# Performance work log

Hardware: AMD Instinct MI355X
Metric: run time of the kernel (lower is better)

The kernel has to match this reference:

```python
import jax, jax.numpy as jnp
import numpy as np
from jax import lax

B, S, D, NH, K = 4, 2048, 1024, 16, 3
EPS = 1e-6


def custom_layernorm(x, gamma, beta):
    # torch-style: std with ddof=1, eps added to std (not var)
    mean = jnp.mean(x, axis=-1, keepdims=True)
    var = jnp.sum((x - mean) ** 2, axis=-1, keepdims=True) / (x.shape[-1] - 1)
    std = jnp.sqrt(var)
    return gamma * ((x - mean) / (std + EPS)) + beta


def setup_inputs() -> dict:
    key = jax.random.key(0)
    ks = jax.random.split(key, 10)
    s = 1.0 / np.sqrt(D)
    return {
        "x": jax.random.normal(ks[0], (B, S, D), jnp.float32),
        "Wq": jax.random.normal(ks[1], (D, D), jnp.float32) * s,
        "bq": jax.random.normal(ks[2], (D,), jnp.float32) * 0.02,
        "Wk": jax.random.normal(ks[3], (D, D), jnp.float32) * s,
        "Wv": jax.random.normal(ks[4], (D, D), jnp.float32) * s,
        "bv": jax.random.normal(ks[5], (D,), jnp.float32) * 0.02,
        "conv_w": jax.random.normal(ks[6], (D, D // NH, K), jnp.float32) * (1.0 / np.sqrt((D // NH) * K)),
        "conv_b": jax.random.normal(ks[7], (D,), jnp.float32) * 0.02,
        "gamma": jnp.ones((D,), jnp.float32),
        "beta": jnp.zeros((D,), jnp.float32),
        "Wo": jax.random.normal(ks[8], (D, D), jnp.float32) * s,
        "bo": jax.random.normal(ks[9], (D,), jnp.float32) * 0.02,
    }


def reference(x, Wq, bq, Wk, Wv, bv, conv_w, conv_b, gamma, beta, Wo, bo):
    d = x.shape[-1]
    groups = d // conv_w.shape[1]
    pad = conv_w.shape[2] // 2

    q = x @ Wq + bq
    k = x @ Wk  # key has no bias
    v = x @ Wv + bv

    # grouped conv1d over sequence dim (NCW layout)
    xc = jnp.transpose(x, (0, 2, 1))  # [B, D, S]
    conv_out = lax.conv_general_dilated(
        xc, conv_w, window_strides=(1,), padding=[(pad, pad)],
        feature_group_count=groups,
        dimension_numbers=("NCH", "OIH", "NCH"),
    ) + conv_b[None, :, None]
    conv_out = jnp.transpose(conv_out, (0, 2, 1))  # [B, S, D]
    conv_out = custom_layernorm(conv_out, gamma, beta)  # dropout = identity (eval)

    scale = 1.0 / jnp.sqrt(jnp.asarray(d, x.dtype))
    scores = jnp.einsum("bqd,bkd->bqk", q, k) * scale  # [B, S, S]
    attn = jax.nn.softmax(scores, axis=-1)
    attention_out = jnp.einsum("bqk,bkd->bqd", attn, v)

    combined = custom_layernorm(conv_out + attention_out, gamma, beta)
    return combined @ Wo + bo + x
```

## Files before the change

kernel.cpp:

```cpp
#include <hip/hip_runtime.h>
#include <cstdint>


#define DEV __device__ __forceinline__

typedef unsigned short u16;
typedef __attribute__((ext_vector_type(8))) short bf16x8;
typedef __attribute__((ext_vector_type(4))) float f32x4;

static const int Sn = 2048, Dn = 1024;

DEV float bf2f(u16 u) { union { unsigned int i; float f; } w; w.i = ((unsigned int)u) << 16; return w.f; }
DEV u16 f2bf(float f) {
  union { float f; unsigned int i; } w; w.f = f;
  unsigned int x = w.i;
  return (u16)((x + 0x7FFFu + ((x >> 16) & 1u)) >> 16);
}

DEV void gload_lds16(const u16* gsrc, u16* lds_dst) {
  __builtin_amdgcn_global_load_lds(
      (const __attribute__((address_space(1))) void*)gsrc,
      (__attribute__((address_space(3))) void*)lds_dst,
      16, 0, 0);
}

DEV float block_allreduce_sum(float v, float* red, int tid) {
  #pragma unroll
  for (int o = 32; o > 0; o >>= 1) v += __shfl_down(v, o, 64);
  __syncthreads();
  if ((tid & 63) == 0) red[tid >> 6] = v;
  __syncthreads();
  return red[0] + red[1] + red[2] + red[3];
}

DEV float block_allreduce_max(float v, float* red, int tid) {
  #pragma unroll
  for (int o = 32; o > 0; o >>= 1) v = fmaxf(v, __shfl_down(v, o, 64));
  __syncthreads();
  if ((tid & 63) == 0) red[tid >> 6] = v;
  __syncthreads();
  return fmaxf(fmaxf(red[0], red[1]), fmaxf(red[2], red[3]));
}

DEV void ln_row(const u16* __restrict__ a, const u16* __restrict__ b2,
                const float* __restrict__ gamma, const float* __restrict__ beta,
                u16* __restrict__ out, long row, int tid, float* red) {
  long base = row * Dn + tid * 4;
  ushort4 av = *(const ushort4*)&a[base];
  float v0 = bf2f(av.x), v1 = bf2f(av.y), v2 = bf2f(av.z), v3 = bf2f(av.w);
  if (b2) {
    ushort4 bv4 = *(const ushort4*)&b2[base];
    v0 += bf2f(bv4.x); v1 += bf2f(bv4.y); v2 += bf2f(bv4.z); v3 += bf2f(bv4.w);
  }
  float s = block_allreduce_sum(v0 + v1 + v2 + v3, red, tid);
  float mean = s * (1.0f / 1024.0f);
  float d0 = v0 - mean, d1 = v1 - mean, d2 = v2 - mean, d3 = v3 - mean;
  float sq = block_allreduce_sum(d0 * d0 + d1 * d1 + d2 * d2 + d3 * d3, red, tid);
  float inv = 1.0f / (sqrtf(sq * (1.0f / 1023.0f)) + 1e-6f);
  float4 gv = *(const float4*)&gamma[tid * 4];
  float4 bev = *(const float4*)&beta[tid * 4];
  ushort4 o;
  o.x = f2bf(gv.x * d0 * inv + bev.x);
  o.y = f2bf(gv.y * d1 * inv + bev.y);
  o.z = f2bf(gv.z * d2 * inv + bev.z);
  o.w = f2bf(gv.w * d3 * inv + bev.w);
  *(ushort4*)&out[base] = o;
}

__global__ __launch_bounds__(256)
void prep_all(const float* __restrict__ Wq, const float* __restrict__ Wk,
              const float* __restrict__ Wv, const float* __restrict__ Wo,
              u16* __restrict__ wT,
              const float* __restrict__ bq, const float* __restrict__ bv,
              float* __restrict__ qkvb,
              const float* __restrict__ x, u16* __restrict__ xb) {
  __shared__ u16 sm[64][68];
  int blk = blockIdx.x;
  int tid = threadIdx.x;
  if (blk < 1024) {
    int w = blk >> 8, t = blk & 255;
    const float* src = (w == 0) ? Wq : (w == 1) ? Wk : (w == 2) ? Wv : Wo;
    u16* dst = wT + (size_t)w * 1048576u;
    int i0 = (t >> 4) << 6, j0 = (t & 15) << 6;
    int tx = tid & 15, r0 = tid >> 4;
    #pragma unroll
    for (int rr = r0; rr < 64; rr += 16) {
      float4 v = *(const float4*)&src[(long)(i0 + rr) * 1024 + j0 + tx * 4];
      sm[rr][tx*4+0] = f2bf(v.x); sm[rr][tx*4+1] = f2bf(v.y);
      sm[rr][tx*4+2] = f2bf(v.z); sm[rr][tx*4+3] = f2bf(v.w);
    }
    __syncthreads();
    #pragma unroll
    for (int cc = r0; cc < 64; cc += 16) {
      ushort4 o;
      o.x = sm[tx*4+0][cc]; o.y = sm[tx*4+1][cc];
      o.z = sm[tx*4+2][cc]; o.w = sm[tx*4+3][cc];
      *(ushort4*)&dst[(long)(j0 + cc) * 1024 + i0 + tx * 4] = o;
    }
  } else if (blk == 1024) {
    for (int j = tid; j < 3072; j += 256) {
      float v = 0.0f;
      if (j < 1024) v = bq[j];
      else if (j >= 2048) v = bv[j - 2048];
      qkvb[j] = v;
    }
  } else {
    int i = (blk - 1025) * 1024 + tid * 4;
    float4 v = *(const float4*)&x[i];
    ushort4 o;
    o.x = f2bf(v.x); o.y = f2bf(v.y); o.z = f2bf(v.z); o.w = f2bf(v.w);
    *(ushort4*)&xb[i] = o;
  }
}

__global__ __launch_bounds__(512, 2)
void gemm8(const u16* __restrict__ A, long Abs, int lda,
           const u16* __restrict__ B, long Bbs, int ldb,
           u16* __restrict__ C0, u16* __restrict__ C1, int zsplit,
           long Cbs, int ldc, int K, float scale,
           const float* __restrict__ bias, int bias_bs) {
  extern __shared__ u16 lds[];
  int tid = threadIdx.x;
  int w = tid >> 6, ln = tid & 63;
  int quad = ln >> 4, lm = ln & 15;
  int wr = w >> 2, wc = w & 3;
  long m0 = (long)blockIdx.x * 256, n0 = (long)blockIdx.y * 256;
  int z = blockIdx.z;
  A += (long)z * Abs;
  B += (long)z * Bbs;
  u16* C = (z < zsplit) ? C0 + (long)z * Cbs : C1 + (long)(z - zsplit) * Cbs;

  int sg = ((ln & 7) ^ (ln >> 3)) * 8;
  int row0 = w * 8 + (ln >> 3);
  const u16* As0 = A + (m0 + row0) * (long)lda + sg;
  const u16* As1 = As0 + 64 * (long)lda;
  const u16* Bs0 = B + (n0 + row0) * (long)ldb + sg;
  const u16* Bs1 = Bs0 + 64 * (long)ldb;
  u16* dA = lds + w * 512;
  u16* dB = lds + 16384 + w * 512;

  int rA = wr * 16 + lm;
  int rB = wc * 16 + lm;
  int g0 = (quad ^ (lm & 7)) * 8;
  int g1 = ((4 + quad) ^ (lm & 7)) * 8;

#define STGA(buf, h, k0) do { \
    gload_lds16(As0 + (long)(h) * 128 * lda + (k0), dA + (buf) * 32768 + (h) * 8192); \
    gload_lds16(As1 + (long)(h) * 128 * lda + (k0), dA + (buf) * 32768 + (h) * 8192 + 4096); } while (0)
#define STGB(buf, h, k0) do { \
    gload_lds16(Bs0 + (long)(h) * 128 * ldb + (k0), dB + (buf) * 32768 + (h) * 8192); \
    gload_lds16(Bs1 + (long)(h) * 128 * ldb + (k0), dB + (buf) * 32768 + (h) * 8192 + 4096); } while (0)
#define LDA_F(ab, mi, kk) (*(const bf16x8*)&lds[(ab) + ((mi) * 32 + rA) * 64 + ((kk) ? g1 : g0)])
#define LDB_F(bb, ni, kk) (*(const bf16x8*)&lds[(bb) + ((ni) * 64 + rB) * 64 + ((kk) ? g1 : g0)])
#define MFMA(a, b, c) __builtin_amdgcn_mfma_f32_16x16x32_bf16(a, b, c, 0, 0, 0)

  f32x4 acc[8][4] = {};
  bf16x8 bfr[4][2];
  int nt = K >> 6;

  STGB(0, 0, 0); STGB(0, 1, 0); STGA(0, 0, 0); STGA(0, 1, 0);
  asm volatile("s_waitcnt vmcnt(2)" ::: "memory");
  __builtin_amdgcn_sched_barrier(0);
  __builtin_amdgcn_s_barrier();

  for (int t = 0; t < nt; ++t) {
    int buf = t & 1;
    int abase = buf * 32768, bbase = abase + 16384;
    int nbuf = buf ^ 1;
    int kn = (t + 1) << 6;
    bool more = (t + 1 < nt);

    {
      #pragma unroll
      for (int ni = 0; ni < 4; ni++) {
        bfr[ni][0] = LDB_F(bbase, ni, 0);
        bfr[ni][1] = LDB_F(bbase, ni, 1);
      }
      bf16x8 a00 = LDA_F(abase, 0, 0), a01 = LDA_F(abase, 0, 1);
      bf16x8 a10 = LDA_F(abase, 1, 0), a11 = LDA_F(abase, 1, 1);
      if (more) STGB(nbuf, 0, kn);
      __builtin_amdgcn_s_barrier();
      __builtin_amdgcn_s_setprio(1);
      #pragma unroll
      for (int ni = 0; ni < 4; ni++) {
        acc[0][ni] = MFMA(a00, bfr[ni][0], acc[0][ni]);
        acc[0][ni] = MFMA(a01, bfr[ni][1], acc[0][ni]);
        acc[1][ni] = MFMA(a10, bfr[ni][0], acc[1][ni]);
        acc[1][ni] = MFMA(a11, bfr[ni][1], acc[1][ni]);
      }
      __builtin_amdgcn_s_setprio(0);
      __builtin_amdgcn_s_barrier();
    }
    {
      bf16x8 a00 = LDA_F(abase, 2, 0), a01 = LDA_F(abase, 2, 1);
      bf16x8 a10 = LDA_F(abase, 3, 0), a11 = LDA_F(abase, 3, 1);
      if (more) STGB(nbuf, 1, kn);
      __builtin_amdgcn_s_barrier();
      __builtin_amdgcn_s_setprio(1);
      #pragma unroll
      for (int ni = 0; ni < 4; ni++) {
        acc[2][ni] = MFMA(a00, bfr[ni][0], acc[2][ni]);
        acc[2][ni] = MFMA(a01, bfr[ni][1], acc[2][ni]);
        acc[3][ni] = MFMA(a10, bfr[ni][0], acc[3][ni]);
        acc[3][ni] = MFMA(a11, bfr[ni][1], acc[3][ni]);
      }
      __builtin_amdgcn_s_setprio(0);
      if (more) asm volatile("s_waitcnt vmcnt(4)" ::: "memory");
      else      asm volatile("s_waitcnt vmcnt(0)" ::: "memory");
      __builtin_amdgcn_sched_barrier(0);
      __builtin_amdgcn_s_barrier();
    }
    {
      bf16x8 a00 = LDA_F(abase, 4, 0), a01 = LDA_F(abase, 4, 1);
      bf16x8 a10 = LDA_F(abase, 5, 0), a11 = LDA_F(abase, 5, 1);
      if (more) STGA(nbuf, 0, kn);
      __builtin_amdgcn_s_barrier();
      __builtin_amdgcn_s_setprio(1);
      #pragma unroll
      for (int ni = 0; ni < 4; ni++) {
        acc[4][ni] = MFMA(a00, bfr[ni][0], acc[4][ni]);
        acc[4][ni] = MFMA(a01, bfr[ni][1], acc[4][ni]);
        acc[5][ni] = MFMA(a10, bfr[ni][0], acc[5][ni]);
        acc[5][ni] = MFMA(a11, bfr[ni][1], acc[5][ni]);
      }
      __builtin_amdgcn_s_setprio(0);
      __builtin_amdgcn_s_barrier();
    }
    {
      bf16x8 a00 = LDA_F(abase, 6, 0), a01 = LDA_F(abase, 6, 1);
      bf16x8 a10 = LDA_F(abase, 7, 0), a11 = LDA_F(abase, 7, 1);
      if (more) STGA(nbuf, 1, kn);
      __builtin_amdgcn_s_barrier();
      __builtin_amdgcn_s_setprio(1);
      #pragma unroll
      for (int ni = 0; ni < 4; ni++) {
        acc[6][ni] = MFMA(a00, bfr[ni][0], acc[6][ni]);
        acc[6][ni] = MFMA(a01, bfr[ni][1], acc[6][ni]);
        acc[7][ni] = MFMA(a10, bfr[ni][0], acc[7][ni]);
        acc[7][ni] = MFMA(a11, bfr[ni][1], acc[7][ni]);
      }
      __builtin_amdgcn_s_setprio(0);
      if (more) {
        asm volatile("s_waitcnt vmcnt(2)" ::: "memory");
        __builtin_amdgcn_sched_barrier(0);
      }
      __builtin_amdgcn_s_barrier();
    }
  }

  #pragma unroll
  for (int mi = 0; mi < 8; mi++) {
    #pragma unroll
    for (int ni = 0; ni < 4; ni++) {
      int col = (int)n0 + ni * 64 + wc * 16 + lm;
      float bvv = bias ? bias[(long)z * bias_bs + col] : 0.0f;
      #pragma unroll
      for (int r = 0; r < 4; r++) {
        long rowg = m0 + mi * 32 + wr * 16 + quad * 4 + r;
        C[rowg * (long)ldc + col] = f2bf(acc[mi][ni][r] * scale + bvv);
      }
    }
  }
#undef STGA
#undef STGB
#undef LDA_F
#undef LDB_F
#undef MFMA
}

template<typename CT>
__global__ __launch_bounds__(256, 2)
void gemm_nt(const u16* __restrict__ A, const u16* __restrict__ A2, long Abs, int lda,
             const u16* __restrict__ B, long Bbs, int ldb,
             CT* __restrict__ C, CT* __restrict__ C2, long Cbs, int ldc,
             int zsplit, int K, float scale,
             const float* __restrict__ bias, int bias_bs,
             const float* __restrict__ res, long Rbs, int ldr) {
  __shared__ u16 sA[2][128 * 32];
  __shared__ u16 sB[2][128 * 32];
  int tid = threadIdx.x;
  int lane = tid & 63, wv = tid >> 6;
  int quad = lane >> 4, lm = lane & 15;
  int wr = wv >> 1, wc = wv & 1;
  long m0 = (long)blockIdx.x * 128, n0 = (long)blockIdx.y * 128;
  int z = blockIdx.z;
  if (z >= zsplit) { A = A2 + (long)(z - zsplit) * Abs; C = C2 + (long)(z - zsplit) * Cbs; }
  else             { A = A  + (long)z * Abs;            C = C  + (long)z * Cbs; }
  B += (long)z * Bbs;
  if (res) res += (long)z * Rbs;

  f32x4 acc[4][4] = {};

  int srow = wv * 16 + (lane >> 2);
  int sch = (lane & 3) * 8;
  const u16* Ap = A + (m0 + srow) * (long)lda + sch;
  const u16* Bp = B + (n0 + srow) * (long)ldb + sch;
  const int lofs = wv * 16 * 32;

  for (int k0 = 0; k0 < K; k0 += 64) {
    #pragma unroll
    for (int h = 0; h < 2; h++) {
      int kh = k0 + h * 32;
      gload_lds16(Ap + kh, &sA[h][lofs]);
      gload_lds16(Ap + 64 * (long)lda + kh, &sA[h][lofs + 64 * 32]);
      gload_lds16(Bp + kh, &sB[h][lofs]);
      gload_lds16(Bp + 64 * (long)ldb + kh, &sB[h][lofs + 64 * 32]);
    }
    __syncthreads();
    #pragma unroll
    for (int h = 0; h < 2; h++) {
      bf16x8 af[4], bfr[4];
      #pragma unroll
      for (int mi = 0; mi < 4; mi++)
        af[mi] = *(const bf16x8*)&sA[h][(wr * 64 + mi * 16 + lm) * 32 + quad * 8];
      #pragma unroll
      for (int ni = 0; ni < 4; ni++)
        bfr[ni] = *(const bf16x8*)&sB[h][(wc * 64 + ni * 16 + lm) * 32 + quad * 8];
      #pragma unroll
      for (int mi = 0; mi < 4; mi++)
        #pragma unroll
        for (int ni = 0; ni < 4; ni++)
          acc[mi][ni] = __builtin_amdgcn_mfma_f32_16x16x32_bf16(af[mi], bfr[ni], acc[mi][ni], 0, 0, 0);
    }
    __syncthreads();
  }

  #pragma unroll
  for (int mi = 0; mi < 4; mi++) {
    #pragma unroll
    for (int ni = 0; ni < 4; ni++) {
      int col = (int)n0 + wc * 64 + ni * 16 + lm;
      float bv = bias ? bias[(long)z * bias_bs + col] : 0.0f;
      #pragma unroll
      for (int r = 0; r < 4; r++) {
        long rowg = m0 + wr * 64 + mi * 16 + quad * 4 + r;
        float v = acc[mi][ni][r] * scale + bv;
        if (res) v += res[rowg * (long)ldr + col];
        if constexpr (sizeof(CT) == 2) C[rowg * (long)ldc + col] = f2bf(v);
        else                           C[rowg * (long)ldc + col] = v;
      }
    }
  }
}

__global__ __launch_bounds__(256, 2)
void post_qkv(int ngemm,
              const u16* __restrict__ Qb, const u16* __restrict__ Kb,
              u16* __restrict__ Pd, u16* __restrict__ Pw,
              const u16* __restrict__ Vb, u16* __restrict__ vt) {
  __shared__ u16 smem[2 * 2 * 128 * 32];
  int blk = blockIdx.x;
  int tid = threadIdx.x;
  if (blk < ngemm) {
    u16* sA0 = smem;
    u16* sB0 = smem + 2 * 128 * 32;
    int lane = tid & 63, wv = tid >> 6;
    int quad = lane >> 4, lm = lane & 15;
    int wr = wv >> 1, wc = wv & 1;
    int z = blk >> 8;
    long m0 = (long)(blk & 15) * 128, n0 = (long)((blk >> 4) & 15) * 128;
    const u16* A = Qb + (long)z * Sn * Dn;
    const u16* B = Kb + (long)z * Sn * Dn;
    u16* C = (z < 2) ? Pd + (long)z * Sn * Sn : Pw + (long)(z - 2) * Sn * Sn;

    f32x4 acc[4][4] = {};
    int srow = wv * 16 + (lane >> 2);
    int sch = (lane & 3) * 8;
    const u16* Ap = A + (m0 + srow) * 1024 + sch;
    const u16* Bp = B + (n0 + srow) * 1024 + sch;
    const int lofs = wv * 16 * 32;

    for (int k0 = 0; k0 < 1024; k0 += 64) {
      #pragma unroll
      for (int h = 0; h < 2; h++) {
        int kh = k0 + h * 32;
        gload_lds16(Ap + kh, &sA0[h * 128 * 32 + lofs]);
        gload_lds16(Ap + 64 * 1024 + kh, &sA0[h * 128 * 32 + lofs + 64 * 32]);
        gload_lds16(Bp + kh, &sB0[h * 128 * 32 + lofs]);
        gload_lds16(Bp + 64 * 1024 + kh, &sB0[h * 128 * 32 + lofs + 64 * 32]);
      }
      __syncthreads();
      #pragma unroll
      for (int h = 0; h < 2; h++) {
        bf16x8 af[4], bfr[4];
        #pragma unroll
        for (int mi = 0; mi < 4; mi++)
          af[mi] = *(const bf16x8*)&sA0[h * 128 * 32 + (wr * 64 + mi * 16 + lm) * 32 + quad * 8];
        #pragma unroll
        for (int ni = 0; ni < 4; ni++)
          bfr[ni] = *(const bf16x8*)&sB0[h * 128 * 32 + (wc * 64 + ni * 16 + lm) * 32 + quad * 8];
        #pragma unroll
        for (int mi = 0; mi < 4; mi++)
          #pragma unroll
          for (int ni = 0; ni < 4; ni++)
            acc[mi][ni] = __builtin_amdgcn_mfma_f32_16x16x32_bf16(af[mi], bfr[ni], acc[mi][ni], 0, 0, 0);
      }
      __syncthreads();
    }
    #pragma unroll
    for (int mi = 0; mi < 4; mi++) {
      #pragma unroll
      for (int ni = 0; ni < 4; ni++) {
        int col = (int)n0 + wc * 64 + ni * 16 + lm;
        #pragma unroll
        for (int r = 0; r < 4; r++) {
          long rowg = m0 + wr * 64 + mi * 16 + quad * 4 + r;
          C[rowg * 2048 + col] = f2bf(acc[mi][ni][r] * 0.03125f);
        }
      }
    }
  } else {
    u16 (*sm)[68] = (u16(*)[68])smem;
    int t = blk - ngemm;
    int b = t >> 9, r = t & 511;
    int j0 = (r & 15) << 6, i0 = ((r >> 4) & 31) << 6;
    const u16* s = Vb + (long)b * Sn * Dn;
    u16* d = vt + (long)b * Dn * Sn;
    int tx = tid & 15, r0 = tid >> 4;
    #pragma unroll
    for (int rr = r0; rr < 64; rr += 16) {
      ushort4 v = *(const ushort4*)&s[(long)(i0 + rr) * 1024 + j0 + tx * 4];
      sm[rr][tx*4+0] = v.x; sm[rr][tx*4+1] = v.y; sm[rr][tx*4+2] = v.z; sm[rr][tx*4+3] = v.w;
    }
    __syncthreads();
    #pragma unroll
    for (int cc = r0; cc < 64; cc += 16) {
      ushort4 o;
      o.x = sm[tx*4+0][cc]; o.y = sm[tx*4+1][cc];
      o.z = sm[tx*4+2][cc]; o.w = sm[tx*4+3][cc];
      *(ushort4*)&d[(long)(j0 + cc) * 2048 + i0 + tx * 4] = o;
    }
  }
}

__global__ __launch_bounds__(256)
void smax_conv(u16* __restrict__ pa, u16* __restrict__ pb, int rowsplit,
               int nsm, int nconv,
               const float* __restrict__ x, const float* __restrict__ cw,
               const float* __restrict__ cb, u16* __restrict__ convo,
               const u16* __restrict__ Vb, u16* __restrict__ vt) {
  __shared__ u16 smem[22160];
  __shared__ float red[4];
  int blk = blockIdx.x;
  int tid = threadIdx.x;
  if (blk < nsm) {
    long row = blk;
    u16* p = (row < rowsplit) ? pa + row * 2048 : pb + (row - rowsplit) * 2048;
    ushort4 a = *(const ushort4*)&p[tid * 8];
    ushort4 b = *(const ushort4*)&p[tid * 8 + 4];
    float f0 = bf2f(a.x), f1 = bf2f(a.y), f2 = bf2f(a.z), f3 = bf2f(a.w);
    float f4 = bf2f(b.x), f5 = bf2f(b.y), f6 = bf2f(b.z), f7 = bf2f(b.w);
    float m = fmaxf(fmaxf(fmaxf(f0, f1), fmaxf(f2, f3)),
                    fmaxf(fmaxf(f4, f5), fmaxf(f6, f7)));
    m = block_allreduce_max(m, red, tid);
    float e0 = __expf(f0 - m), e1 = __expf(f1 - m), e2 = __expf(f2 - m), e3 = __expf(f3 - m);
    float e4 = __expf(f4 - m), e5 = __expf(f5 - m), e6 = __expf(f6 - m), e7 = __expf(f7 - m);
    float s = block_allreduce_sum(e0 + e1 + e2 + e3 + e4 + e5 + e6 + e7, red, tid);
    float inv = 1.0f / s;
    ushort4 o1, o2;
    o1.x = f2bf(e0 * inv); o1.y = f2bf(e1 * inv); o1.z = f2bf(e2 * inv); o1.w = f2bf(e3 * inv);
    o2.x = f2bf(e4 * inv); o2.y = f2bf(e5 * inv); o2.z = f2bf(e6 * inv); o2.w = f2bf(e7 * inv);
    *(ushort4*)&p[tid * 8] = o1;
    *(ushort4*)&p[tid * 8 + 4] = o2;
  } else if (blk < nsm + nconv) {
    u16 (*sx)[72] = (u16(*)[72])smem;
    u16 (*sw)[200] = (u16(*)[200])(smem + 9360);
    int r = blk - nsm;
    int s0 = (r & 15) * 128;
    int g = (r >> 4) & 15;
    int b = r >> 8;
    int lane = tid & 63, wv = tid >> 6;
    int quad = lane >> 4, lm = lane & 15;
    for (int idx = tid; idx < 64 * 192; idx += 256) {
      int oc = idx / 192, k = idx - oc * 192;
      int t = k >> 6, i = k & 63;
      sw[oc][k] = f2bf(cw[((long)(g * 64 + oc)) * 192 + i * 3 + t]);
    }
    for (int idx = tid; idx < 130 * 16; idx += 256) {
      int rr = idx >> 4, c4 = (idx & 15) * 4;
      int s = s0 - 1 + rr;
      ushort4 v;
      if (s >= 0 && s < Sn) {
        float4 f = *(const float4*)&x[((long)b * Sn + s) * Dn + g * 64 + c4];
        v.x = f2bf(f.x); v.y = f2bf(f.y); v.z = f2bf(f.z); v.w = f2bf(f.w);
      } else { v.x = 0; v.y = 0; v.z = 0; v.w = 0; }
      *(ushort4*)&sx[rr][c4] = v;
    }
    __syncthreads();
    f32x4 acc[2][4] = {};
    #pragma unroll
    for (int ks = 0; ks < 6; ks++) {
      int t = ks >> 1;
      int i0 = (ks & 1) * 32 + quad * 8;
      bf16x8 a0 = *(const bf16x8*)&sx[wv * 32 + lm + t][i0];
      bf16x8 a1 = *(const bf16x8*)&sx[wv * 32 + 16 + lm + t][i0];
      #pragma unroll
      for (int nf = 0; nf < 4; nf++) {
        bf16x8 bf = *(const bf16x8*)&sw[nf * 16 + lm][ks * 32 + quad * 8];
        acc[0][nf] = __builtin_amdgcn_mfma_f32_16x16x32_bf16(a0, bf, acc[0][nf], 0, 0, 0);
        acc[1][nf] = __builtin_amdgcn_mfma_f32_16x16x32_bf16(a1, bf, acc[1][nf], 0, 0, 0);
      }
    }
    #pragma unroll
    for (int mi = 0; mi < 2; mi++) {
      #pragma unroll
      for (int nf = 0; nf < 4; nf++) {
        int col = g * 64 + nf * 16 + lm;
        float bias = cb[col];
        #pragma unroll
        for (int rr = 0; rr < 4; rr++) {
          int row = wv * 32 + mi * 16 + quad * 4 + rr;
          convo[((long)b * Sn + s0 + row) * Dn + col] = f2bf(acc[mi][nf][rr] + bias);
        }
      }
    }
  } else {
    u16 (*sm)[68] = (u16(*)[68])smem;
    int t = blk - nsm - nconv;
    int b = t >> 9, r = t & 511;
    int j0 = (r & 15) << 6, i0 = ((r >> 4) & 31) << 6;
    const u16* s = Vb + (long)b * Sn * Dn;
    u16* d = vt + (long)b * Dn * Sn;
    int tx = tid & 15, r0 = tid >> 4;
    #pragma unroll
    for (int rr = r0; rr < 64; rr += 16) {
      ushort4 v = *(const ushort4*)&s[(long)(i0 + rr) * 1024 + j0 + tx * 4];
      sm[rr][tx*4+0] = v.x; sm[rr][tx*4+1] = v.y; sm[rr][tx*4+2] = v.z; sm[rr][tx*4+3] = v.w;
    }
    __syncthreads();
    #pragma unroll
    for (int cc = r0; cc < 64; cc += 16) {
      ushort4 o;
      o.x = sm[tx*4+0][cc]; o.y = sm[tx*4+1][cc];
      o.z = sm[tx*4+2][cc]; o.w = sm[tx*4+3][cc];
      *(ushort4*)&d[(long)(j0 + cc) * 2048 + i0 + tx * 4] = o;
    }
  }
}

__global__ __launch_bounds__(256, 2)
void pv_ln(int npv,
           const u16* __restrict__ Pd, const u16* __restrict__ Pw,
           const u16* __restrict__ vt, u16* __restrict__ attn,
           u16* __restrict__ conv,
           const float* __restrict__ gamma, const float* __restrict__ beta) {
  __shared__ u16 smem[2 * 2 * 128 * 32];
  __shared__ float red[4];
  int blk = blockIdx.x;
  int tid = threadIdx.x;
  if (blk < npv) {
    u16* sA0 = smem;
    u16* sB0 = smem + 2 * 128 * 32;
    int lane = tid & 63, wv = tid >> 6;
    int quad = lane >> 4, lm = lane & 15;
    int wr = wv >> 1, wc = wv & 1;
    int z = blk >> 7;
    long m0 = (long)(blk & 15) * 128, n0 = (long)((blk >> 4) & 7) * 128;
    const u16* A = (z < 2) ? Pd + (long)z * Sn * Sn : Pw + (long)(z - 2) * Sn * Sn;
    const u16* B = vt + (long)z * Dn * Sn;
    u16* C = attn + (long)z * Sn * Dn;

    f32x4 acc[4][4] = {};
    int srow = wv * 16 + (lane >> 2);
    int sch = (lane & 3) * 8;
    const u16* Ap = A + (m0 + srow) * 2048 + sch;
    const u16* Bp = B + (n0 + srow) * 2048 + sch;
    const int lofs = wv * 16 * 32;

    for (int k0 = 0; k0 < 2048; k0 += 64) {
      #pragma unroll
      for (int h = 0; h < 2; h++) {
        int kh = k0 + h * 32;
        gload_lds16(Ap + kh, &sA0[h * 128 * 32 + lofs]);
        gload_lds16(Ap + 64 * 2048 + kh, &sA0[h * 128 * 32 + lofs + 64 * 32]);
        gload_lds16(Bp + kh, &sB0[h * 128 * 32 + lofs]);
        gload_lds16(Bp + 64 * 2048 + kh, &sB0[h * 128 * 32 + lofs + 64 * 32]);
      }
      __syncthreads();
      #pragma unroll
      for (int h = 0; h < 2; h++) {
        bf16x8 af[4], bfr[4];
        #pragma unroll
        for (int mi = 0; mi < 4; mi++)
          af[mi] = *(const bf16x8*)&sA0[h * 128 * 32 + (wr * 64 + mi * 16 + lm) * 32 + quad * 8];
        #pragma unroll
        for (int ni = 0; ni < 4; ni++)
          bfr[ni] = *(const bf16x8*)&sB0[h * 128 * 32 + (wc * 64 + ni * 16 + lm) * 32 + quad * 8];
        #pragma unroll
        for (int mi = 0; mi < 4; mi++)
          #pragma unroll
          for (int ni = 0; ni < 4; ni++)
            acc[mi][ni] = __builtin_amdgcn_mfma_f32_16x16x32_bf16(af[mi], bfr[ni], acc[mi][ni], 0, 0, 0);
      }
      __syncthreads();
    }
    #pragma unroll
    for (int mi = 0; mi < 4; mi++) {
      #pragma unroll
      for (int ni = 0; ni < 4; ni++) {
        int col = (int)n0 + wc * 64 + ni * 16 + lm;
        #pragma unroll
        for (int r = 0; r < 4; r++) {
          long rowg = m0 + wr * 64 + mi * 16 + quad * 4 + r;
          C[rowg * 1024 + col] = f2bf(acc[mi][ni][r]);
        }
      }
    }
  } else {
    long row = blk - npv;
    ln_row(conv, nullptr, gamma, beta, conv, row, tid, red);
  }
}

__global__ __launch_bounds__(256)
void ln_kernel(const u16* __restrict__ a, const u16* __restrict__ b2,
               const float* __restrict__ gamma, const float* __restrict__ beta,
               u16* __restrict__ out) {
  __shared__ float red[4];
  ln_row(a, b2, gamma, beta, out, blockIdx.x, threadIdx.x, red);
}

static const size_t OFF_WT    = 0;
static const size_t OFF_QKVB  = 8ull << 20;
static const size_t OFF_Q     = 9ull << 20;
static const size_t OFF_K     = 25ull << 20;
static const size_t OFF_V     = 41ull << 20;
static const size_t OFF_PW    = 57ull << 20;

extern "C" void kernel_launch(void* const* d_in, const int* in_sizes, int n_in,
                              void* d_out, int out_size, void* d_ws, size_t ws_size,
                              hipStream_t stream) {
  const float* x     = (const float*)d_in[0];
  const float* Wq    = (const float*)d_in[1];
  const float* bq    = (const float*)d_in[2];
  const float* Wk    = (const float*)d_in[3];
  const float* Wv    = (const float*)d_in[4];
  const float* bv    = (const float*)d_in[5];
  const float* cw    = (const float*)d_in[6];
  const float* cb    = (const float*)d_in[7];
  const float* gamma = (const float*)d_in[8];
  const float* beta  = (const float*)d_in[9];
  const float* Wo    = (const float*)d_in[10];
  const float* bo    = (const float*)d_in[11];
  float* out = (float*)d_out;
  char* ws = (char*)d_ws;

  u16*   wT    = (u16*)(ws + OFF_WT);
  float* qkvb  = (float*)(ws + OFF_QKVB);
  u16*   Qb    = (u16*)(ws + OFF_Q);
  u16*   Kb    = (u16*)(ws + OFF_K);
  u16*   Vb    = (u16*)(ws + OFF_V);
  u16*   Pw    = (u16*)(ws + OFF_PW);
  u16*   xb    = (u16*)d_out;
  u16*   Pd    = (u16*)d_out;
  u16*   vt    = (u16*)d_out + 8388608;
  u16*   attn  = Qb;
  u16*   combined = Kb;
  const long PBS = (long)Sn * Sn;

  static int gemm8_attr = 0;
  if (!gemm8_attr) {
    hipFuncSetAttribute((const void*)gemm8,
                        hipFuncAttributeMaxDynamicSharedMemorySize, 131072);
    gemm8_attr = 1;
  }

  dim3 tb(256);
  dim3 tb8(512);

  prep_all<<<dim3(9217), tb, 0, stream>>>(Wq, Wk, Wv, Wo, wT, bq, bv, qkvb, x, xb);
  gemm8<<<dim3(32, 4, 3), tb8, 131072, stream>>>(
      xb, 0, 1024, wT, 1048576, 1024,
      Qb, (u16*)nullptr, 99, 8388608, 1024,
      1024, 1.0f, qkvb, 1024);

  if (ws_size >= (73ull << 20)) {
    u16* conv = Kb;
    gemm8<<<dim3(8, 8, 4), tb8, 131072, stream>>>(
        Qb, (long)Sn * Dn, 1024, Kb, (long)Sn * Dn, 1024,
        Pd, Pw, 2, PBS, 2048,
        1024, 0.03125f, nullptr, 0);
    smax_conv<<<dim3(8192 + 1024 + 2048), tb, 0, stream>>>(
        Pd, Pw, 4096, 8192, 1024, x, cw, cb, conv, Vb, vt);
    pv_ln<<<dim3(512 + 8192), tb, 0, stream>>>(512, Pd, Pw, vt, attn, conv,
                                               gamma, beta);
    ln_kernel<<<dim3(8192), tb, 0, stream>>>(conv, attn, gamma, beta, combined);
  } else {
    u16* conv = Vb;
    post_qkv<<<dim3(2048), tb, 0, stream>>>(0, Qb, Kb, Pd, Pw, Vb, vt);
    for (int c = 0; c < 2; c++) {
      long off = (long)c * 2 * Sn * Dn;
      gemm_nt<u16><<<dim3(16, 16, 2), tb, 0, stream>>>(
          Qb + off, nullptr, (long)Sn * Dn, 1024, Kb + off, (long)Sn * Dn, 1024,
          Pd, (u16*)nullptr, PBS, 2048,
          99, 1024, 0.03125f, nullptr, 0, nullptr, 0, 0);
      smax_conv<<<dim3(4096 + (c == 0 ? 1024 : 0)), tb, 0, stream>>>(
          Pd, Pd, 4096, 4096, (c == 0 ? 1024 : 0), x, cw, cb, conv, Vb, vt);
      gemm_nt<u16><<<dim3(16, 8, 2), tb, 0, stream>>>(
          Pd, nullptr, PBS, 2048, vt + off, (long)Dn * Sn, 2048,
          attn + off, (u16*)nullptr, (long)Sn * Dn, 1024,
          99, 2048, 1.0f, nullptr, 0, nullptr, 0, 0);
    }
    ln_kernel<<<dim3(8192), tb, 0, stream>>>(conv, nullptr, gamma, beta, conv);
    ln_kernel<<<dim3(8192), tb, 0, stream>>>(conv, attn, gamma, beta, combined);
  }

  gemm_nt<float><<<dim3(64, 8, 1), tb, 0, stream>>>(
      combined, nullptr, 0, 1024, wT + 3u * 1048576u, 0, 1024,
      out, (float*)nullptr, 0, 1024,
      99, 1024, 1.0f, bo, 0, x, 0, 1024);
}
```

Measured before the change: 365.0 us.

## Software-pipeline gemm8 fragment loads across iterations and vectorize transposed epilogue stores

Restructures the gemm8 main loop so A fragments ping-pong between two register sets and the next tile's first A/B fragments are prefetched from LDS before the last MFMA cluster. Global-to-LDS staging is reordered with adjusted vmcnt waits. MFMA operands are swapped so the accumulators hold a transposed tile, which lets the epilogue use float4 bias loads and ushort4 stores instead of scalar stores. It adds register pressure and tighter synchronization ordering.

```diff
diff --git a/kernel.cpp b/kernel.cpp
--- a/kernel.cpp
+++ b/kernel.cpp
@@ -119,7 +119,8 @@
            u16* __restrict__ C0, u16* __restrict__ C1, int zsplit,
            long Cbs, int ldc, int K, float scale,
            const float* __restrict__ bias, int bias_bs) {
-  extern __shared__ u16 lds[];
+  extern __shared__ ulong2 lds_raw[];
+  u16* lds = (u16*)lds_raw;
   int tid = threadIdx.x;
   int w = tid >> 6, ln = tid & 63;
   int quad = ln >> 4, lm = ln & 15;
@@ -153,112 +154,105 @@
 #define LDA_F(ab, mi, kk) (*(const bf16x8*)&lds[(ab) + ((mi) * 32 + rA) * 64 + ((kk) ? g1 : g0)])
 #define LDB_F(bb, ni, kk) (*(const bf16x8*)&lds[(bb) + ((ni) * 64 + rB) * 64 + ((kk) ? g1 : g0)])
 #define MFMA(a, b, c) __builtin_amdgcn_mfma_f32_16x16x32_bf16(a, b, c, 0, 0, 0)
+#define CLUSTER(S, MLO, MHI) do { \
+    _Pragma("unroll") \
+    for (int ni = 0; ni < 4; ni++) { \
+      acc[MLO][ni] = MFMA(bfr[ni][0], S[0], acc[MLO][ni]); \
+      acc[MLO][ni] = MFMA(bfr[ni][1], S[1], acc[MLO][ni]); \
+      acc[MHI][ni] = MFMA(bfr[ni][0], S[2], acc[MHI][ni]); \
+      acc[MHI][ni] = MFMA(bfr[ni][1], S[3], acc[MHI][ni]); \
+    } } while (0)
+#define RDA(dst, base, mi) do { \
+    dst[0] = LDA_F(base, mi, 0); dst[1] = LDA_F(base, mi, 1); \
+    dst[2] = LDA_F(base, (mi) + 1, 0); dst[3] = LDA_F(base, (mi) + 1, 1); } while (0)
+#define VMCNT(n) do { asm volatile("s_waitcnt vmcnt(" #n ")" ::: "memory"); \
+    __builtin_amdgcn_sched_barrier(0); } while (0)
+#define BAR() __builtin_amdgcn_s_barrier()
 
   f32x4 acc[8][4] = {};
   bf16x8 bfr[4][2];
+  bf16x8 nb0[2], nb1[2];
+  bf16x8 aE[4], aO[4];
   int nt = K >> 6;
 
-  STGB(0, 0, 0); STGB(0, 1, 0); STGA(0, 0, 0); STGA(0, 1, 0);
-  asm volatile("s_waitcnt vmcnt(2)" ::: "memory");
-  __builtin_amdgcn_sched_barrier(0);
-  __builtin_amdgcn_s_barrier();
+  STGA(0, 0, 0); STGB(0, 0, 0); STGB(0, 1, 0); STGA(0, 1, 0);
+  VMCNT(4);
+  BAR();
+  {
+    RDA(aE, 0, 0);
+    bfr[0][0] = LDB_F(16384, 0, 0); bfr[0][1] = LDB_F(16384, 0, 1);
+    bfr[1][0] = LDB_F(16384, 1, 0); bfr[1][1] = LDB_F(16384, 1, 1);
+  }
+  VMCNT(2);
+  BAR();
 
   for (int t = 0; t < nt; ++t) {
     int buf = t & 1;
     int abase = buf * 32768, bbase = abase + 16384;
     int nbuf = buf ^ 1;
+    int nbabase = nbuf * 32768, nbbbase = nbabase + 16384;
     int kn = (t + 1) << 6;
     bool more = (t + 1 < nt);
 
-    {
-      #pragma unroll
-      for (int ni = 0; ni < 4; ni++) {
-        bfr[ni][0] = LDB_F(bbase, ni, 0);
-        bfr[ni][1] = LDB_F(bbase, ni, 1);
-      }
-      bf16x8 a00 = LDA_F(abase, 0, 0), a01 = LDA_F(abase, 0, 1);
-      bf16x8 a10 = LDA_F(abase, 1, 0), a11 = LDA_F(abase, 1, 1);
-      if (more) STGB(nbuf, 0, kn);
-      __builtin_amdgcn_s_barrier();
-      __builtin_amdgcn_s_setprio(1);
-      #pragma unroll
-      for (int ni = 0; ni < 4; ni++) {
-        acc[0][ni] = MFMA(a00, bfr[ni][0], acc[0][ni]);
-        acc[0][ni] = MFMA(a01, bfr[ni][1], acc[0][ni]);
-        acc[1][ni] = MFMA(a10, bfr[ni][0], acc[1][ni]);
-        acc[1][ni] = MFMA(a11, bfr[ni][1], acc[1][ni]);
-      }
-      __builtin_amdgcn_s_setprio(0);
-      __builtin_amdgcn_s_barrier();
-    }
-    {
-      bf16x8 a00 = LDA_F(abase, 2, 0), a01 = LDA_F(abase, 2, 1);
-      bf16x8 a10 = LDA_F(abase, 3, 0), a11 = LDA_F(abase, 3, 1);
-      if (more) STGB(nbuf, 1, kn);
-      __builtin_amdgcn_s_barrier();
-      __builtin_amdgcn_s_setprio(1);
-      #pragma unroll
-      for (int ni = 0; ni < 4; ni++) {
-        acc[2][ni] = MFMA(a00, bfr[ni][0], acc[2][ni]);
-        acc[2][ni] = MFMA(a01, bfr[ni][1], acc[2][ni]);
-        acc[3][ni] = MFMA(a10, bfr[ni][0], acc[3][ni]);
-        acc[3][ni] = MFMA(a11, bfr[ni][1], acc[3][ni]);
-      }
-      __builtin_amdgcn_s_setprio(0);
-      if (more) asm volatile("s_waitcnt vmcnt(4)" ::: "memory");
-      else      asm volatile("s_waitcnt vmcnt(0)" ::: "memory");
-      __builtin_amdgcn_sched_barrier(0);
-      __builtin_amdgcn_s_barrier();
-    }
-    {
-      bf16x8 a00 = LDA_F(abase, 4, 0), a01 = LDA_F(abase, 4, 1);
-      bf16x8 a10 = LDA_F(abase, 5, 0), a11 = LDA_F(abase, 5, 1);
-      if (more) STGA(nbuf, 0, kn);
-      __builtin_amdgcn_s_barrier();
-      __builtin_amdgcn_s_setprio(1);
-      #pragma unroll
-      for (int ni = 0; ni < 4; ni++) {
-        acc[4][ni] = MFMA(a00, bfr[ni][0], acc[4][ni]);
-        acc[4][ni] = MFMA(a01, bfr[ni][1], acc[4][ni]);
-        acc[5][ni] = MFMA(a10, bfr[ni][0], acc[5][ni]);
-        acc[5][ni] = MFMA(a11, bfr[ni][1], acc[5][ni]);
-      }
-      __builtin_amdgcn_s_setprio(0);
-      __builtin_amdgcn_s_barrier();
-    }
-    {
-      bf16x8 a00 = LDA_F(abase, 6, 0), a01 = LDA_F(abase, 6, 1);
-      bf16x8 a10 = LDA_F(abase, 7, 0), a11 = LDA_F(abase, 7, 1);
-      if (more) STGA(nbuf, 1, kn);
-      __builtin_amdgcn_s_barrier();
-      __builtin_amdgcn_s_setprio(1);
-      #pragma unroll
-      for (int ni = 0; ni < 4; ni++) {
-        acc[6][ni] = MFMA(a00, bfr[ni][0], acc[6][ni]);
-        acc[6][ni] = MFMA(a01, bfr[ni][1], acc[6][ni]);
-        acc[7][ni] = MFMA(a10, bfr[ni][0], acc[7][ni]);
-        acc[7][ni] = MFMA(a11, bfr[ni][1], acc[7][ni]);
-      }
-      __builtin_amdgcn_s_setprio(0);
-      if (more) {
-        asm volatile("s_waitcnt vmcnt(2)" ::: "memory");
-        __builtin_amdgcn_sched_barrier(0);
-      }
-      __builtin_amdgcn_s_barrier();
+    bfr[2][0] = LDB_F(bbase, 2, 0); bfr[2][1] = LDB_F(bbase, 2, 1);
+    bfr[3][0] = LDB_F(bbase, 3, 0); bfr[3][1] = LDB_F(bbase, 3, 1);
+    RDA(aO, abase, 2);
+    if (more) STGA(nbuf, 0, kn);
+    BAR();
+    __builtin_amdgcn_s_setprio(1);
+    CLUSTER(aE, 0, 1);
+    __builtin_amdgcn_s_setprio(0);
+    if (more) VMCNT(2); else VMCNT(0);
+    BAR();
+    RDA(aE, abase, 4);
+    if (more) STGB(nbuf, 0, kn);
+    BAR();
+    __builtin_amdgcn_s_setprio(1);
+    CLUSTER(aO, 2, 3);
+    __builtin_amdgcn_s_setprio(0);
+    BAR();
+    RDA(aO, abase, 6);
+    if (more) STGB(nbuf, 1, kn);
+    BAR();
+    __builtin_amdgcn_s_setprio(1);
+    CLUSTER(aE, 4, 5);
+    __builtin_amdgcn_s_setprio(0);
+    if (more) VMCNT(2);
+    BAR();
+    if (more) {
+      RDA(aE, nbabase, 0);
+      nb0[0] = LDB_F(nbbbase, 0, 0); nb0[1] = LDB_F(nbbbase, 0, 1);
+      nb1[0] = LDB_F(nbbbase, 1, 0); nb1[1] = LDB_F(nbbbase, 1, 1);
+      STGA(nbuf, 1, kn);
+    }
+    BAR();
+    __builtin_amdgcn_s_setprio(1);
+    CLUSTER(aO, 6, 7);
+    __builtin_amdgcn_s_setprio(0);
+    if (more) VMCNT(2);
+    BAR();
+    if (more) {
+      bfr[0][0] = nb0[0]; bfr[0][1] = nb0[1];
+      bfr[1][0] = nb1[0]; bfr[1][1] = nb1[1];
     }
   }
 
   #pragma unroll
   for (int mi = 0; mi < 8; mi++) {
+    long m = m0 + mi * 32 + wr * 16 + lm;
+    u16* Crow = C + m * (long)ldc;
     #pragma unroll
     for (int ni = 0; ni < 4; ni++) {
-      int col = (int)n0 + ni * 64 + wc * 16 + lm;
-      float bvv = bias ? bias[(long)z * bias_bs + col] : 0.0f;
-      #pragma unroll
-      for (int r = 0; r < 4; r++) {
-        long rowg = m0 + mi * 32 + wr * 16 + quad * 4 + r;
-        C[rowg * (long)ldc + col] = f2bf(acc[mi][ni][r] * scale + bvv);
-      }
+      int nb = (int)n0 + ni * 64 + wc * 16 + quad * 4;
+      float4 bv4;
+      if (bias) bv4 = *(const float4*)&bias[(long)z * bias_bs + nb];
+      else      bv4 = float4{0.0f, 0.0f, 0.0f, 0.0f};
+      ushort4 o;
+      o.x = f2bf(acc[mi][ni][0] * scale + bv4.x);
+      o.y = f2bf(acc[mi][ni][1] * scale + bv4.y);
+      o.z = f2bf(acc[mi][ni][2] * scale + bv4.z);
+      o.w = f2bf(acc[mi][ni][3] * scale + bv4.w);
+      *(ushort4*)&Crow[nb] = o;
     }
   }
 #undef STGA
@@ -266,6 +260,10 @@
 #undef LDA_F
 #undef LDB_F
 #undef MFMA
+#undef CLUSTER
+#undef RDA
+#undef VMCNT
+#undef BAR
 }
 
 template<typename CT>
```

Result: slower. 374.6 us (+2.6%).
